# Kernel tuning notes

Measured on AMD Instinct MI355X. Metric: run time of the kernel, lower is better.

The kernel has to match this reference:

```python
import jax, jax.numpy as jnp
import numpy as np


def _make_coord(n):
    # grid-center coords in (-1, 1), matching make_coord in the torch code
    return -1.0 + 1.0 / n + (2.0 / n) * jnp.arange(n, dtype=jnp.float32)


def _mlp(inp, W1, b1, W2, b2, W3, b3):
    h = jax.nn.relu(inp @ W1 + b1)
    h = jax.nn.relu(h @ W2 + b2)
    return h @ W3 + b3


def setup_inputs() -> dict:
    key = jax.random.key(0)
    ks = jax.random.split(key, 4)
    dim = 64
    x = jax.random.normal(ks[0], (4, dim, 64, 64), dtype=jnp.float32)
    W1 = jax.random.normal(ks[1], (dim + 2, 256), dtype=jnp.float32) * 0.05
    W2 = jax.random.normal(ks[2], (256, 256), dtype=jnp.float32) * 0.05
    W3 = jax.random.normal(ks[3], (256, dim), dtype=jnp.float32) * 0.05
    return {
        "x": x,
        "W1": W1, "b1": jnp.zeros((256,), jnp.float32),
        "W2": W2, "b2": jnp.zeros((256,), jnp.float32),
        "W3": W3, "b3": jnp.zeros((dim,), jnp.float32),
        "h_out": 256, "w_out": 256,
    }


def reference(x, W1, b1, W2, b2, W3, b3, h_out, w_out):
    B, C, H, W = x.shape
    # query coords on the output grid (same for every batch element)
    gy, gx = jnp.meshgrid(_make_coord(h_out), _make_coord(w_out), indexing="ij")
    cy = gy.reshape(-1)  # [Q], coord channel 0 (height)
    cx = gx.reshape(-1)  # [Q], coord channel 1 (width)
    rx = 1.0 / H  # = 2 / H / 2
    ry = 1.0 / W
    eps_shift = 1e-6
    lim = 1.0 - 1e-6
    fy = _make_coord(H)  # feat_coord values along height
    fx = _make_coord(W)

    preds = []
    areas = []
    for vx in (-1.0, 1.0):
        for vy in (-1.0, 1.0):
            sy = jnp.clip(cy + vx * rx + eps_shift, -lim, lim)
            sx = jnp.clip(cx + vy * ry + eps_shift, -lim, lim)
            # grid_sample nearest, align_corners=False: unnormalize then round
            iy = jnp.clip(jnp.round(((sy + 1.0) * H - 1.0) * 0.5), 0, H - 1).astype(jnp.int32)
            ix = jnp.clip(jnp.round(((sx + 1.0) * W - 1.0) * 0.5), 0, W - 1).astype(jnp.int32)
            q_feat = x[:, :, iy, ix].transpose(0, 2, 1)  # [B, Q, C]
            rel_y = (cy - fy[iy]) * H  # [Q]
            rel_x = (cx - fx[ix]) * W
            rel = jnp.stack([rel_y, rel_x], axis=-1)  # [Q, 2]
            inp = jnp.concatenate(
                [q_feat, jnp.broadcast_to(rel, (B,) + rel.shape)], axis=-1
            )  # [B, Q, C+2]
            preds.append(_mlp(inp, W1, b1, W2, b2, W3, b3))  # [B, Q, C]
            areas.append(jnp.abs(rel_y * rel_x) + 1e-9)  # [Q]

    tot_area = areas[0] + areas[1] + areas[2] + areas[3]
    # local_ensemble swap: 0<->3, 1<->2 (opposite-corner area weighting)
    areas = [areas[3], areas[2], areas[1], areas[0]]
    ret = 0.0
    for pred, area in zip(preds, areas):
        ret = ret + pred * (area / tot_area)[None, :, None]
    return ret  # [B, h_out*w_out, C]
```

## Files before the change

### kernel.cpp

```cpp
#include <hip/hip_runtime.h>


typedef __bf16 bf16x8 __attribute__((ext_vector_type(8)));
typedef float  f32x4  __attribute__((ext_vector_type(4)));
typedef unsigned int u32x2 __attribute__((ext_vector_type(2)));

#define LDS_SWZ(row, kbyte) ((kbyte) ^ (((row) & 7) << 4))

#define WP1_U 0
#define WP2_U (48 * 512)
#define WP3_U (176 * 512)
#define XT_OFF (1 << 20)

__global__ __launch_bounds__(64) void prep_weights(
    const float* __restrict__ W1, const float* __restrict__ W2,
    const float* __restrict__ W3, ushort* __restrict__ ws)
{
    const int blk = blockIdx.x;
    const int l   = threadIdx.x;
    const float* W; int Kreal, N, ks, nt; size_t off;
    if (blk < 48)       { W = W1; Kreal = 66;  N = 256; ks = blk >> 4;  nt = blk & 15; off = WP1_U + (size_t)blk * 512; }
    else if (blk < 176) { int b2 = blk - 48;  W = W2; Kreal = 256; N = 256; ks = b2 >> 4; nt = b2 & 15; off = WP2_U + (size_t)b2 * 512; }
    else                { int b3 = blk - 176; W = W3; Kreal = 256; N = 64;  ks = b3 >> 2; nt = b3 & 3;  off = WP3_U + (size_t)b3 * 512; }

    const int n = nt * 16 + (l & 15);
    ushort v[8];
    #pragma unroll
    for (int j = 0; j < 8; ++j) {
        const int k = ks * 32 + ((l >> 4) * 8) + j;
        const float f = (k < Kreal) ? W[(size_t)k * N + n] : 0.0f;
        v[j] = __builtin_bit_cast(ushort, (__bf16)f);
    }
    *(uint4*)(ws + off + (size_t)l * 8) = *(const uint4*)v;
}

__global__ __launch_bounds__(256) void prep_xt(const float* __restrict__ x, char* __restrict__ xt)
{
    const int blk = blockIdx.x;
    const int b = blk >> 6, iy = blk & 63;
    const int ix = threadIdx.x & 63, cq = threadIdx.x >> 6;
    ushort v[16];
    #pragma unroll
    for (int j = 0; j < 16; ++j) {
        const int ch = cq * 16 + j;
        const float f = x[(((size_t)b * 64 + ch) * 64 + iy) * 64 + ix];
        v[j] = __builtin_bit_cast(ushort, (__bf16)f);
    }
    char* dst = xt + ((size_t)((b * 4096 + iy * 64 + ix)) * 128) + cq * 32;
    *(uint4*)dst        = *(const uint4*)(v);
    *(uint4*)(dst + 16) = *(const uint4*)(v + 8);
}

__device__ inline unsigned pk2(float a, float b) {
    return (unsigned)__builtin_bit_cast(ushort, (__bf16)a)
         | ((unsigned)__builtin_bit_cast(ushort, (__bf16)b) << 16);
}

template<int KSTEPS>
__device__ inline void compute_layer_T(const char* __restrict__ src,
                                       const ushort* __restrict__ wp,
                                       const float* __restrict__ bias,
                                       int lane, int wtile4, f32x4 (&acc)[4][4])
{
    const int lrow = lane & 15;
    const int lk   = lane >> 4;
    #pragma unroll
    for (int mt = 0; mt < 4; ++mt) {
        const f32x4 bs = *(const f32x4*)(bias + (wtile4 + mt) * 16 + lk * 4);
        #pragma unroll
        for (int nt = 0; nt < 4; ++nt) acc[mt][nt] = bs;
    }
    const ushort* wpl = wp + ((size_t)wtile4 << 9) + (lane << 3);
    #pragma unroll 1
    for (int ks = 0; ks < KSTEPS; ++ks) {
        bf16x8 wa[4];
        #pragma unroll
        for (int mt = 0; mt < 4; ++mt)
            wa[mt] = *(const bf16x8*)(wpl + ((size_t)(ks * 16 + mt) << 9));
        #pragma unroll
        for (int nt = 0; nt < 4; ++nt) {
            const int row   = nt * 16 + lrow;
            const int kbyte = ks * 64 + lk * 16;
            const bf16x8 hb = *(const bf16x8*)(src + row * 512 + LDS_SWZ(row, kbyte));
            __builtin_amdgcn_s_setprio(1);
            #pragma unroll
            for (int mt = 0; mt < 4; ++mt)
                acc[mt][nt] = __builtin_amdgcn_mfma_f32_16x16x32_bf16(wa[mt], hb, acc[mt][nt], 0, 0, 0);
            __builtin_amdgcn_s_setprio(0);
        }
    }
}

__device__ inline void store_hidden_T(char* __restrict__ dst, const f32x4 (&acc)[4][4],
                                      int lane, int wtile4)
{
    const int lrow = lane & 15;
    const int lk   = lane >> 4;
    #pragma unroll
    for (int nt = 0; nt < 4; ++nt) {
        const int row = nt * 16 + lrow;
        #pragma unroll
        for (int mt = 0; mt < 4; ++mt) {
            const int nb = ((wtile4 + mt) * 16 + lk * 4) * 2;
            u32x2 p;
            p[0] = pk2(fmaxf(acc[mt][nt][0], 0.0f), fmaxf(acc[mt][nt][1], 0.0f));
            p[1] = pk2(fmaxf(acc[mt][nt][2], 0.0f), fmaxf(acc[mt][nt][3], 0.0f));
            *(u32x2*)(dst + row * 512 + LDS_SWZ(row, nb)) = p;
        }
    }
}

__global__ __launch_bounds__(256, 3) void liif_mfma10_kernel(
    const char* __restrict__ xt,
    const float* __restrict__ b1f, const float* __restrict__ b2f, const float* __restrict__ b3f,
    const ushort* __restrict__ ws, float* __restrict__ out)
{
    __shared__ char bufH[32 * 1024];

    const int tid  = threadIdx.x;
    const int lane = tid & 63;
    const int wv   = tid >> 6;
    const int lrow = lane & 15;
    const int lk   = lane >> 4;
    const int wtile4 = wv * 4;

    const int bid0 = blockIdx.x;
    const int b    = (bid0 & 7) >> 1;
    const int qidx = (bid0 >> 3) * 2 + (bid0 & 1);
    const int q0   = qidx << 4;

    int   pix_off[4];
    float rely[4], relx[4], wgt[4];
    {
        const int q  = q0 + lrow;
        const int yq = q >> 8, xq = q & 255;
        const float cy  = -1.0f + (2.0f * yq + 1.0f) / 256.0f;
        const float cx  = -1.0f + (2.0f * xq + 1.0f) / 256.0f;
        const float lim = 1.0f - 1e-6f;
        float area[4];
        #pragma unroll
        for (int c = 0; c < 4; ++c) {
            const float vx = (c & 2) ? 1.0f : -1.0f;
            const float vy = (c & 1) ? 1.0f : -1.0f;
            float sy = cy + vx * (1.0f / 64.0f) + 1e-6f;
            float sx = cx + vy * (1.0f / 64.0f) + 1e-6f;
            sy = fminf(fmaxf(sy, -lim), lim);
            sx = fminf(fmaxf(sx, -lim), lim);
            int iyv = (int)rintf(((sy + 1.0f) * 64.0f - 1.0f) * 0.5f);
            int ixv = (int)rintf(((sx + 1.0f) * 64.0f - 1.0f) * 0.5f);
            iyv = min(max(iyv, 0), 63);
            ixv = min(max(ixv, 0), 63);
            const float fy = -1.0f + (2.0f * iyv + 1.0f) / 64.0f;
            const float fx = -1.0f + (2.0f * ixv + 1.0f) / 64.0f;
            rely[c] = (cy - fy) * 64.0f;
            relx[c] = (cx - fx) * 64.0f;
            pix_off[c] = (b * 4096 + iyv * 64 + ixv) * 128;
            area[c] = fabsf(rely[c] * relx[c]) + 1e-9f;
        }
        const float tot = area[0] + area[1] + area[2] + area[3];
        #pragma unroll
        for (int c = 0; c < 4; ++c) wgt[c] = area[3 - c] / tot;
    }

    f32x4 acc[4][4];

    {
        #pragma unroll
        for (int mt = 0; mt < 4; ++mt) {
            const f32x4 bs = *(const f32x4*)(b1f + (wtile4 + mt) * 16 + lk * 4);
            #pragma unroll
            for (int nt = 0; nt < 4; ++nt) acc[mt][nt] = bs;
        }
        const ushort* wpl = ws + WP1_U + ((size_t)wtile4 << 9) + (lane << 3);
        #pragma unroll 1
        for (int ks = 0; ks < 2; ++ks) {
            bf16x8 wa[4];
            #pragma unroll
            for (int mt = 0; mt < 4; ++mt)
                wa[mt] = *(const bf16x8*)(wpl + ((size_t)(ks * 16 + mt) << 9));
            #pragma unroll
            for (int nt = 0; nt < 4; ++nt) {
                const bf16x8 hb = *(const bf16x8*)(xt + pix_off[nt] + ks * 64 + lk * 16);
                __builtin_amdgcn_s_setprio(1);
                #pragma unroll
                for (int mt = 0; mt < 4; ++mt)
                    acc[mt][nt] = __builtin_amdgcn_mfma_f32_16x16x32_bf16(wa[mt], hb, acc[mt][nt], 0, 0, 0);
                __builtin_amdgcn_s_setprio(0);
            }
        }
        {
            bf16x8 wa[4];
            #pragma unroll
            for (int mt = 0; mt < 4; ++mt)
                wa[mt] = *(const bf16x8*)(wpl + ((size_t)(32 + mt) << 9));
            #pragma unroll
            for (int nt = 0; nt < 4; ++nt) {
                bf16x8 hb = (bf16x8){0, 0, 0, 0, 0, 0, 0, 0};
                if (lk == 0) { hb[0] = (__bf16)rely[nt]; hb[1] = (__bf16)relx[nt]; }
                __builtin_amdgcn_s_setprio(1);
                #pragma unroll
                for (int mt = 0; mt < 4; ++mt)
                    acc[mt][nt] = __builtin_amdgcn_mfma_f32_16x16x32_bf16(wa[mt], hb, acc[mt][nt], 0, 0, 0);
                __builtin_amdgcn_s_setprio(0);
            }
        }
    }
    store_hidden_T(bufH, acc, lane, wtile4);
    __syncthreads();

    compute_layer_T<8>(bufH, ws + WP2_U, b2f, lane, wtile4, acc);
    __syncthreads();
    store_hidden_T(bufH, acc, lane, wtile4);
    __syncthreads();

    {
        f32x4 acc3[4];
        const f32x4 bs3 = *(const f32x4*)(b3f + wv * 16 + lk * 4);
        #pragma unroll
        for (int mt = 0; mt < 4; ++mt) acc3[mt] = bs3;

        const ushort* wp3 = ws + WP3_U + (lane << 3);
        #pragma unroll 1
        for (int ks = 0; ks < 8; ++ks) {
            const bf16x8 wa = *(const bf16x8*)(wp3 + ((size_t)(ks * 4 + wv) << 9));
            #pragma unroll
            for (int mt = 0; mt < 4; ++mt) {
                const int row   = mt * 16 + lrow;
                const int kbyte = ks * 64 + lk * 16;
                const bf16x8 hb = *(const bf16x8*)(bufH + row * 512 + LDS_SWZ(row, kbyte));
                __builtin_amdgcn_s_setprio(1);
                acc3[mt] = __builtin_amdgcn_mfma_f32_16x16x32_bf16(wa, hb, acc3[mt], 0, 0, 0);
                __builtin_amdgcn_s_setprio(0);
            }
        }
        __syncthreads();
        #pragma unroll
        for (int mt = 0; mt < 4; ++mt) {
            const int row = mt * 16 + lrow;
            const f32x4 v = acc3[mt] * wgt[mt];
            const int cb = wv * 64 + lk * 16;
            *(f32x4*)(bufH + row * 256 + LDS_SWZ(row, cb)) = v;
        }
    }
    __syncthreads();

    {
        const int q  = tid >> 4;
        const int ch = (tid & 15) * 4;
        f32x4 sum = (f32x4){0.f, 0.f, 0.f, 0.f};
        #pragma unroll
        for (int c = 0; c < 4; ++c) {
            const int row = c * 16 + q;
            const f32x4 v = *(const f32x4*)(bufH + row * 256 + LDS_SWZ(row, ch * 4));
            sum += v;
        }
        *(f32x4*)(out + ((size_t)b * 65536 + q0 + q) * 64 + ch) = sum;
    }
}

extern "C" void kernel_launch(void* const* d_in, const int* in_sizes, int n_in,
                              void* d_out, int out_size, void* d_ws, size_t ws_size,
                              hipStream_t stream) {
    const float* x  = (const float*)d_in[0];
    const float* W1 = (const float*)d_in[1];
    const float* b1 = (const float*)d_in[2];
    const float* W2 = (const float*)d_in[3];
    const float* b2 = (const float*)d_in[4];
    const float* W3 = (const float*)d_in[5];
    const float* b3 = (const float*)d_in[6];
    float* out = (float*)d_out;
    ushort* wp = (ushort*)d_ws;
    char* xt   = (char*)d_ws + XT_OFF;

    prep_weights<<<208, 64, 0, stream>>>(W1, W2, W3, wp);
    prep_xt<<<256, 256, 0, stream>>>(x, xt);
    liif_mfma10_kernel<<<16384, 256, 0, stream>>>(xt, b1, b2, b3, wp, out);
}
```

Baseline: 236.5 us.

## Split MLP output tiles across eight waves per block instead of four

The block size doubles from 256 to 512 threads, so each wave now owns two 16-column output tiles instead of four in layers 1 and 2. Layer 3 is split by column tile and by half of the 64 rows, and only the first 256 threads do the final reduction. The aim is more waves to hide latency and fewer accumulator registers per wave. In exchange, each B-fragment read from LDS now feeds only two MFMAs instead of four, which doubles LDS read traffic relative to math, and the larger blocks change how many fit on each CU.

```diff
diff --git a/kernel.cpp b/kernel.cpp
--- a/kernel.cpp
+++ b/kernel.cpp
@@ -60,22 +60,22 @@
 __device__ inline void compute_layer_T(const char* __restrict__ src,
                                        const ushort* __restrict__ wp,
                                        const float* __restrict__ bias,
-                                       int lane, int wtile4, f32x4 (&acc)[4][4])
+                                       int lane, int wtile2, f32x4 (&acc)[2][4])
 {
     const int lrow = lane & 15;
     const int lk   = lane >> 4;
     #pragma unroll
-    for (int mt = 0; mt < 4; ++mt) {
-        const f32x4 bs = *(const f32x4*)(bias + (wtile4 + mt) * 16 + lk * 4);
+    for (int mt = 0; mt < 2; ++mt) {
+        const f32x4 bs = *(const f32x4*)(bias + (wtile2 + mt) * 16 + lk * 4);
         #pragma unroll
         for (int nt = 0; nt < 4; ++nt) acc[mt][nt] = bs;
     }
-    const ushort* wpl = wp + ((size_t)wtile4 << 9) + (lane << 3);
+    const ushort* wpl = wp + ((size_t)wtile2 << 9) + (lane << 3);
     #pragma unroll 1
     for (int ks = 0; ks < KSTEPS; ++ks) {
-        bf16x8 wa[4];
-        #pragma unroll
-        for (int mt = 0; mt < 4; ++mt)
+        bf16x8 wa[2];
+        #pragma unroll
+        for (int mt = 0; mt < 2; ++mt)
             wa[mt] = *(const bf16x8*)(wpl + ((size_t)(ks * 16 + mt) << 9));
         #pragma unroll
         for (int nt = 0; nt < 4; ++nt) {
@@ -84,15 +84,15 @@
             const bf16x8 hb = *(const bf16x8*)(src + row * 512 + LDS_SWZ(row, kbyte));
             __builtin_amdgcn_s_setprio(1);
             #pragma unroll
-            for (int mt = 0; mt < 4; ++mt)
+            for (int mt = 0; mt < 2; ++mt)
                 acc[mt][nt] = __builtin_amdgcn_mfma_f32_16x16x32_bf16(wa[mt], hb, acc[mt][nt], 0, 0, 0);
             __builtin_amdgcn_s_setprio(0);
         }
     }
 }
 
-__device__ inline void store_hidden_T(char* __restrict__ dst, const f32x4 (&acc)[4][4],
-                                      int lane, int wtile4)
+__device__ inline void store_hidden_T(char* __restrict__ dst, const f32x4 (&acc)[2][4],
+                                      int lane, int wtile2)
 {
     const int lrow = lane & 15;
     const int lk   = lane >> 4;
@@ -100,8 +100,8 @@
     for (int nt = 0; nt < 4; ++nt) {
         const int row = nt * 16 + lrow;
         #pragma unroll
-        for (int mt = 0; mt < 4; ++mt) {
-            const int nb = ((wtile4 + mt) * 16 + lk * 4) * 2;
+        for (int mt = 0; mt < 2; ++mt) {
+            const int nb = ((wtile2 + mt) * 16 + lk * 4) * 2;
             u32x2 p;
             p[0] = pk2(fmaxf(acc[mt][nt][0], 0.0f), fmaxf(acc[mt][nt][1], 0.0f));
             p[1] = pk2(fmaxf(acc[mt][nt][2], 0.0f), fmaxf(acc[mt][nt][3], 0.0f));
@@ -110,7 +110,7 @@
     }
 }
 
-__global__ __launch_bounds__(256, 3) void liif_mfma10_kernel(
+__global__ __launch_bounds__(512, 2) void liif_mfma11_kernel(
     const char* __restrict__ xt,
     const float* __restrict__ b1f, const float* __restrict__ b2f, const float* __restrict__ b3f,
     const ushort* __restrict__ ws, float* __restrict__ out)
@@ -122,7 +122,7 @@
     const int wv   = tid >> 6;
     const int lrow = lane & 15;
     const int lk   = lane >> 4;
-    const int wtile4 = wv * 4;
+    const int wtile2 = wv * 2;
 
     const int bid0 = blockIdx.x;
     const int b    = (bid0 & 7) >> 1;
@@ -162,36 +162,36 @@
         for (int c = 0; c < 4; ++c) wgt[c] = area[3 - c] / tot;
     }
 
-    f32x4 acc[4][4];
+    f32x4 acc[2][4];
 
     {
         #pragma unroll
-        for (int mt = 0; mt < 4; ++mt) {
-            const f32x4 bs = *(const f32x4*)(b1f + (wtile4 + mt) * 16 + lk * 4);
+        for (int mt = 0; mt < 2; ++mt) {
+            const f32x4 bs = *(const f32x4*)(b1f + (wtile2 + mt) * 16 + lk * 4);
             #pragma unroll
             for (int nt = 0; nt < 4; ++nt) acc[mt][nt] = bs;
         }
-        const ushort* wpl = ws + WP1_U + ((size_t)wtile4 << 9) + (lane << 3);
+        const ushort* wpl = ws + WP1_U + ((size_t)wtile2 << 9) + (lane << 3);
         #pragma unroll 1
         for (int ks = 0; ks < 2; ++ks) {
-            bf16x8 wa[4];
-            #pragma unroll
-            for (int mt = 0; mt < 4; ++mt)
+            bf16x8 wa[2];
+            #pragma unroll
+            for (int mt = 0; mt < 2; ++mt)
                 wa[mt] = *(const bf16x8*)(wpl + ((size_t)(ks * 16 + mt) << 9));
             #pragma unroll
             for (int nt = 0; nt < 4; ++nt) {
                 const bf16x8 hb = *(const bf16x8*)(xt + pix_off[nt] + ks * 64 + lk * 16);
                 __builtin_amdgcn_s_setprio(1);
                 #pragma unroll
-                for (int mt = 0; mt < 4; ++mt)
+                for (int mt = 0; mt < 2; ++mt)
                     acc[mt][nt] = __builtin_amdgcn_mfma_f32_16x16x32_bf16(wa[mt], hb, acc[mt][nt], 0, 0, 0);
                 __builtin_amdgcn_s_setprio(0);
             }
         }
         {
-            bf16x8 wa[4];
-            #pragma unroll
-            for (int mt = 0; mt < 4; ++mt)
+            bf16x8 wa[2];
+            #pragma unroll
+            for (int mt = 0; mt < 2; ++mt)
                 wa[mt] = *(const bf16x8*)(wpl + ((size_t)(32 + mt) << 9));
             #pragma unroll
             for (int nt = 0; nt < 4; ++nt) {
@@ -199,33 +199,35 @@
                 if (lk == 0) { hb[0] = (__bf16)rely[nt]; hb[1] = (__bf16)relx[nt]; }
                 __builtin_amdgcn_s_setprio(1);
                 #pragma unroll
-                for (int mt = 0; mt < 4; ++mt)
+                for (int mt = 0; mt < 2; ++mt)
                     acc[mt][nt] = __builtin_amdgcn_mfma_f32_16x16x32_bf16(wa[mt], hb, acc[mt][nt], 0, 0, 0);
                 __builtin_amdgcn_s_setprio(0);
             }
         }
     }
-    store_hidden_T(bufH, acc, lane, wtile4);
-    __syncthreads();
-
-    compute_layer_T<8>(bufH, ws + WP2_U, b2f, lane, wtile4, acc);
-    __syncthreads();
-    store_hidden_T(bufH, acc, lane, wtile4);
+    store_hidden_T(bufH, acc, lane, wtile2);
+    __syncthreads();
+
+    compute_layer_T<8>(bufH, ws + WP2_U, b2f, lane, wtile2, acc);
+    __syncthreads();
+    store_hidden_T(bufH, acc, lane, wtile2);
     __syncthreads();
 
     {
-        f32x4 acc3[4];
-        const f32x4 bs3 = *(const f32x4*)(b3f + wv * 16 + lk * 4);
-        #pragma unroll
-        for (int mt = 0; mt < 4; ++mt) acc3[mt] = bs3;
+        const int nt3 = wv >> 1;
+        const int mh  = wv & 1;
+        f32x4 acc3[2];
+        const f32x4 bs3 = *(const f32x4*)(b3f + nt3 * 16 + lk * 4);
+        #pragma unroll
+        for (int mt = 0; mt < 2; ++mt) acc3[mt] = bs3;
 
         const ushort* wp3 = ws + WP3_U + (lane << 3);
         #pragma unroll 1
         for (int ks = 0; ks < 8; ++ks) {
-            const bf16x8 wa = *(const bf16x8*)(wp3 + ((size_t)(ks * 4 + wv) << 9));
-            #pragma unroll
-            for (int mt = 0; mt < 4; ++mt) {
-                const int row   = mt * 16 + lrow;
+            const bf16x8 wa = *(const bf16x8*)(wp3 + ((size_t)(ks * 4 + nt3) << 9));
+            #pragma unroll
+            for (int mt = 0; mt < 2; ++mt) {
+                const int row   = (mh * 2 + mt) * 16 + lrow;
                 const int kbyte = ks * 64 + lk * 16;
                 const bf16x8 hb = *(const bf16x8*)(bufH + row * 512 + LDS_SWZ(row, kbyte));
                 __builtin_amdgcn_s_setprio(1);
@@ -235,16 +237,16 @@
         }
         __syncthreads();
         #pragma unroll
-        for (int mt = 0; mt < 4; ++mt) {
-            const int row = mt * 16 + lrow;
-            const f32x4 v = acc3[mt] * wgt[mt];
-            const int cb = wv * 64 + lk * 16;
+        for (int mt = 0; mt < 2; ++mt) {
+            const int row = (mh * 2 + mt) * 16 + lrow;
+            const f32x4 v = acc3[mt] * wgt[mh * 2 + mt];
+            const int cb = nt3 * 64 + lk * 16;
             *(f32x4*)(bufH + row * 256 + LDS_SWZ(row, cb)) = v;
         }
     }
     __syncthreads();
 
-    {
+    if (tid < 256) {
         const int q  = tid >> 4;
         const int ch = (tid & 15) * 4;
         f32x4 sum = (f32x4){0.f, 0.f, 0.f, 0.f};
@@ -274,5 +276,5 @@
 
     prep_weights<<<208, 64, 0, stream>>>(W1, W2, W3, wp);
     prep_xt<<<256, 256, 0, stream>>>(x, xt);
-    liif_mfma10_kernel<<<16384, 256, 0, stream>>>(xt, b1, b2, b3, wp, out);
-}
+    liif_mfma11_kernel<<<16384, 512, 0, stream>>>(xt, b1, b2, b3, wp, out);
+}
```

Measured after the change: 271.3 us. 14.7% more time.

## Double block tile to 32 queries with 8 waves splitting corner halves

Applied to the files above, without the earlier changes.

Each block now handles 32 query points (128 MLP rows) using 512 threads. Waves are split into two halves, each covering two of the four corner samples across both 16-query groups. The LDS buffer doubles to 64KB and the grid halves, which amortizes per-block setup and sync overhead over more rows. In exchange, occupancy drops to 2 blocks per CU and each block has more waves waiting at every barrier.

```diff
diff --git a/kernel.cpp b/kernel.cpp
--- a/kernel.cpp
+++ b/kernel.cpp
@@ -56,83 +56,32 @@
          | ((unsigned)__builtin_bit_cast(ushort, (__bf16)b) << 16);
 }
 
-template<int KSTEPS>
-__device__ inline void compute_layer_T(const char* __restrict__ src,
-                                       const ushort* __restrict__ wp,
-                                       const float* __restrict__ bias,
-                                       int lane, int wtile4, f32x4 (&acc)[4][4])
-{
-    const int lrow = lane & 15;
-    const int lk   = lane >> 4;
-    #pragma unroll
-    for (int mt = 0; mt < 4; ++mt) {
-        const f32x4 bs = *(const f32x4*)(bias + (wtile4 + mt) * 16 + lk * 4);
-        #pragma unroll
-        for (int nt = 0; nt < 4; ++nt) acc[mt][nt] = bs;
-    }
-    const ushort* wpl = wp + ((size_t)wtile4 << 9) + (lane << 3);
-    #pragma unroll 1
-    for (int ks = 0; ks < KSTEPS; ++ks) {
-        bf16x8 wa[4];
-        #pragma unroll
-        for (int mt = 0; mt < 4; ++mt)
-            wa[mt] = *(const bf16x8*)(wpl + ((size_t)(ks * 16 + mt) << 9));
-        #pragma unroll
-        for (int nt = 0; nt < 4; ++nt) {
-            const int row   = nt * 16 + lrow;
-            const int kbyte = ks * 64 + lk * 16;
-            const bf16x8 hb = *(const bf16x8*)(src + row * 512 + LDS_SWZ(row, kbyte));
-            __builtin_amdgcn_s_setprio(1);
-            #pragma unroll
-            for (int mt = 0; mt < 4; ++mt)
-                acc[mt][nt] = __builtin_amdgcn_mfma_f32_16x16x32_bf16(wa[mt], hb, acc[mt][nt], 0, 0, 0);
-            __builtin_amdgcn_s_setprio(0);
-        }
-    }
-}
-
-__device__ inline void store_hidden_T(char* __restrict__ dst, const f32x4 (&acc)[4][4],
-                                      int lane, int wtile4)
-{
-    const int lrow = lane & 15;
-    const int lk   = lane >> 4;
-    #pragma unroll
-    for (int nt = 0; nt < 4; ++nt) {
-        const int row = nt * 16 + lrow;
-        #pragma unroll
-        for (int mt = 0; mt < 4; ++mt) {
-            const int nb = ((wtile4 + mt) * 16 + lk * 4) * 2;
-            u32x2 p;
-            p[0] = pk2(fmaxf(acc[mt][nt][0], 0.0f), fmaxf(acc[mt][nt][1], 0.0f));
-            p[1] = pk2(fmaxf(acc[mt][nt][2], 0.0f), fmaxf(acc[mt][nt][3], 0.0f));
-            *(u32x2*)(dst + row * 512 + LDS_SWZ(row, nb)) = p;
-        }
-    }
-}
-
-__global__ __launch_bounds__(256, 3) void liif_mfma10_kernel(
+__global__ __launch_bounds__(512, 2) void liif_mfma12_kernel(
     const char* __restrict__ xt,
     const float* __restrict__ b1f, const float* __restrict__ b2f, const float* __restrict__ b3f,
     const ushort* __restrict__ ws, float* __restrict__ out)
 {
-    __shared__ char bufH[32 * 1024];
+    __shared__ char bufH[64 * 1024];
 
     const int tid  = threadIdx.x;
     const int lane = tid & 63;
     const int wv   = tid >> 6;
     const int lrow = lane & 15;
     const int lk   = lane >> 4;
-    const int wtile4 = wv * 4;
+    const int mh   = wv >> 2;
+    const int nq   = wv & 3;
+    const int wtile4 = nq * 4;
 
     const int bid0 = blockIdx.x;
     const int b    = (bid0 & 7) >> 1;
     const int qidx = (bid0 >> 3) * 2 + (bid0 & 1);
-    const int q0   = qidx << 4;
-
-    int   pix_off[4];
-    float rely[4], relx[4], wgt[4];
-    {
-        const int q  = q0 + lrow;
+    const int q0   = qidx << 5;
+
+    int   pixT[4];
+    float relyT[4], relxT[4], wgtT[4];
+    #pragma unroll
+    for (int s = 0; s < 2; ++s) {
+        const int q  = q0 + s * 16 + lrow;
         const int yq = q >> 8, xq = q & 255;
         const float cy  = -1.0f + (2.0f * yq + 1.0f) / 256.0f;
         const float cx  = -1.0f + (2.0f * xq + 1.0f) / 256.0f;
@@ -152,14 +101,24 @@
             ixv = min(max(ixv, 0), 63);
             const float fy = -1.0f + (2.0f * iyv + 1.0f) / 64.0f;
             const float fx = -1.0f + (2.0f * ixv + 1.0f) / 64.0f;
-            rely[c] = (cy - fy) * 64.0f;
-            relx[c] = (cx - fx) * 64.0f;
-            pix_off[c] = (b * 4096 + iyv * 64 + ixv) * 128;
-            area[c] = fabsf(rely[c] * relx[c]) + 1e-9f;
+            const float ry = (cy - fy) * 64.0f;
+            const float rx = (cx - fx) * 64.0f;
+            area[c] = fabsf(ry * rx) + 1e-9f;
+            if ((c >> 1) == mh) {
+                const int nt = ((c & 1) << 1) | s;
+                pixT[nt]  = (b * 4096 + iyv * 64 + ixv) * 128;
+                relyT[nt] = ry;
+                relxT[nt] = rx;
+            }
         }
         const float tot = area[0] + area[1] + area[2] + area[3];
         #pragma unroll
-        for (int c = 0; c < 4; ++c) wgt[c] = area[3 - c] / tot;
+        for (int c = 0; c < 4; ++c) {
+            if ((c >> 1) == mh) {
+                const int nt = ((c & 1) << 1) | s;
+                wgtT[nt] = area[3 - c] / tot;
+            }
+        }
     }
 
     f32x4 acc[4][4];
@@ -180,7 +139,7 @@
                 wa[mt] = *(const bf16x8*)(wpl + ((size_t)(ks * 16 + mt) << 9));
             #pragma unroll
             for (int nt = 0; nt < 4; ++nt) {
-                const bf16x8 hb = *(const bf16x8*)(xt + pix_off[nt] + ks * 64 + lk * 16);
+                const bf16x8 hb = *(const bf16x8*)(xt + pixT[nt] + ks * 64 + lk * 16);
                 __builtin_amdgcn_s_setprio(1);
                 #pragma unroll
                 for (int mt = 0; mt < 4; ++mt)
@@ -196,7 +155,7 @@
             #pragma unroll
             for (int nt = 0; nt < 4; ++nt) {
                 bf16x8 hb = (bf16x8){0, 0, 0, 0, 0, 0, 0, 0};
-                if (lk == 0) { hb[0] = (__bf16)rely[nt]; hb[1] = (__bf16)relx[nt]; }
+                if (lk == 0) { hb[0] = (__bf16)relyT[nt]; hb[1] = (__bf16)relxT[nt]; }
                 __builtin_amdgcn_s_setprio(1);
                 #pragma unroll
                 for (int mt = 0; mt < 4; ++mt)
@@ -205,27 +164,79 @@
             }
         }
     }
-    store_hidden_T(bufH, acc, lane, wtile4);
-    __syncthreads();
-
-    compute_layer_T<8>(bufH, ws + WP2_U, b2f, lane, wtile4, acc);
-    __syncthreads();
-    store_hidden_T(bufH, acc, lane, wtile4);
+    {
+        #pragma unroll
+        for (int nt = 0; nt < 4; ++nt) {
+            const int row = mh * 64 + nt * 16 + lrow;
+            #pragma unroll
+            for (int mt = 0; mt < 4; ++mt) {
+                const int nb = ((wtile4 + mt) * 16 + lk * 4) * 2;
+                u32x2 p;
+                p[0] = pk2(fmaxf(acc[mt][nt][0], 0.0f), fmaxf(acc[mt][nt][1], 0.0f));
+                p[1] = pk2(fmaxf(acc[mt][nt][2], 0.0f), fmaxf(acc[mt][nt][3], 0.0f));
+                *(u32x2*)(bufH + row * 512 + LDS_SWZ(row, nb)) = p;
+            }
+        }
+    }
+    __syncthreads();
+
+    {
+        #pragma unroll
+        for (int mt = 0; mt < 4; ++mt) {
+            const f32x4 bs = *(const f32x4*)(b2f + (wtile4 + mt) * 16 + lk * 4);
+            #pragma unroll
+            for (int nt = 0; nt < 4; ++nt) acc[mt][nt] = bs;
+        }
+        const ushort* wpl = ws + WP2_U + ((size_t)wtile4 << 9) + (lane << 3);
+        #pragma unroll 1
+        for (int ks = 0; ks < 8; ++ks) {
+            bf16x8 wa[4];
+            #pragma unroll
+            for (int mt = 0; mt < 4; ++mt)
+                wa[mt] = *(const bf16x8*)(wpl + ((size_t)(ks * 16 + mt) << 9));
+            #pragma unroll
+            for (int nt = 0; nt < 4; ++nt) {
+                const int row   = mh * 64 + nt * 16 + lrow;
+                const int kbyte = ks * 64 + lk * 16;
+                const bf16x8 hb = *(const bf16x8*)(bufH + row * 512 + LDS_SWZ(row, kbyte));
+                __builtin_amdgcn_s_setprio(1);
+                #pragma unroll
+                for (int mt = 0; mt < 4; ++mt)
+                    acc[mt][nt] = __builtin_amdgcn_mfma_f32_16x16x32_bf16(wa[mt], hb, acc[mt][nt], 0, 0, 0);
+                __builtin_amdgcn_s_setprio(0);
+            }
+        }
+    }
+    __syncthreads();
+    {
+        #pragma unroll
+        for (int nt = 0; nt < 4; ++nt) {
+            const int row = mh * 64 + nt * 16 + lrow;
+            #pragma unroll
+            for (int mt = 0; mt < 4; ++mt) {
+                const int nb = ((wtile4 + mt) * 16 + lk * 4) * 2;
+                u32x2 p;
+                p[0] = pk2(fmaxf(acc[mt][nt][0], 0.0f), fmaxf(acc[mt][nt][1], 0.0f));
+                p[1] = pk2(fmaxf(acc[mt][nt][2], 0.0f), fmaxf(acc[mt][nt][3], 0.0f));
+                *(u32x2*)(bufH + row * 512 + LDS_SWZ(row, nb)) = p;
+            }
+        }
+    }
     __syncthreads();
 
     {
         f32x4 acc3[4];
-        const f32x4 bs3 = *(const f32x4*)(b3f + wv * 16 + lk * 4);
+        const f32x4 bs3 = *(const f32x4*)(b3f + nq * 16 + lk * 4);
         #pragma unroll
         for (int mt = 0; mt < 4; ++mt) acc3[mt] = bs3;
 
         const ushort* wp3 = ws + WP3_U + (lane << 3);
         #pragma unroll 1
         for (int ks = 0; ks < 8; ++ks) {
-            const bf16x8 wa = *(const bf16x8*)(wp3 + ((size_t)(ks * 4 + wv) << 9));
+            const bf16x8 wa = *(const bf16x8*)(wp3 + ((size_t)(ks * 4 + nq) << 9));
             #pragma unroll
             for (int mt = 0; mt < 4; ++mt) {
-                const int row   = mt * 16 + lrow;
+                const int row   = mh * 64 + mt * 16 + lrow;
                 const int kbyte = ks * 64 + lk * 16;
                 const bf16x8 hb = *(const bf16x8*)(bufH + row * 512 + LDS_SWZ(row, kbyte));
                 __builtin_amdgcn_s_setprio(1);
@@ -236,9 +247,9 @@
         __syncthreads();
         #pragma unroll
         for (int mt = 0; mt < 4; ++mt) {
-            const int row = mt * 16 + lrow;
-            const f32x4 v = acc3[mt] * wgt[mt];
-            const int cb = wv * 64 + lk * 16;
+            const int row = mh * 64 + mt * 16 + lrow;
+            const f32x4 v = acc3[mt] * wgtT[mt];
+            const int cb = nq * 64 + lk * 16;
             *(f32x4*)(bufH + row * 256 + LDS_SWZ(row, cb)) = v;
         }
     }
@@ -250,7 +261,7 @@
         f32x4 sum = (f32x4){0.f, 0.f, 0.f, 0.f};
         #pragma unroll
         for (int c = 0; c < 4; ++c) {
-            const int row = c * 16 + q;
+            const int row = c * 32 + q;
             const f32x4 v = *(const f32x4*)(bufH + row * 256 + LDS_SWZ(row, ch * 4));
             sum += v;
         }
@@ -274,5 +285,5 @@
 
     prep_weights<<<208, 64, 0, stream>>>(W1, W2, W3, wp);
     prep_xt<<<256, 256, 0, stream>>>(x, xt);
-    liif_mfma10_kernel<<<16384, 256, 0, stream>>>(xt, b1, b2, b3, wp, out);
-}
+    liif_mfma12_kernel<<<8192, 512, 0, stream>>>(xt, b1, b2, b3, wp, out);
+}
```

Measured after the change: 241.1 us. Within noise of the previous version (+1.9%).
